# Optimization experiments

Measured on AMD Instinct MI355X. Metric: run time of the kernel, lower is better.

## Reference

```python
import jax, jax.numpy as jnp
import numpy as np

BITS = 32
HDC_DIM = 512
IN_SCALE = 23  # 1 + 2*input_window_size, window=11


def setup_inputs() -> dict:
    key = jax.random.key(0)
    k1, k2, k3, k4 = jax.random.split(key, 4)
    B = 2
    D = IN_SCALE * IN_SCALE  # 529
    num_nonzero = int(0.5 * D * HDC_DIM)  # 135424
    return {
        "data_input": jax.random.normal(k1, (B, 4 * IN_SCALE, IN_SCALE), dtype=jnp.float32),
        "structure_input": jax.random.normal(k2, (B, IN_SCALE, IN_SCALE), dtype=jnp.float32),
        "parameters_temp": jax.random.uniform(k3, (IN_SCALE, IN_SCALE), dtype=jnp.float32),
        "non_zero_indices": jax.random.randint(k4, (num_nonzero,), 0, D * HDC_DIM, dtype=jnp.int32),
    }


def _bit_unpack(x_float):
    # view float32 bits as int32, unpack into 0/1 per bit (little-endian bit order),
    # matching torch: x.unsqueeze(-1).bitwise_and(2**arange(bits)).ne(0)
    xi = jax.lax.bitcast_convert_type(x_float, jnp.int32)
    mask = jnp.left_shift(jnp.int32(1), jnp.arange(BITS, dtype=jnp.int32))  # [32], incl. sign bit
    return ((xi[..., None] & mask) != 0).astype(jnp.int32)  # [..., 32]


def reference(data_input, structure_input, parameters_temp, non_zero_indices):
    B = data_input.shape[0]
    n = IN_SCALE
    # channel slices
    r = data_input[:, 0:n, :].reshape(B, -1)            # [B, D]
    g = data_input[:, n:2 * n, :].reshape(B, -1)
    b = data_input[:, 2 * n:3 * n, :].reshape(B, -1)
    a = data_input[:, 3 * n:4 * n, :].reshape(B, -1)
    s = (structure_input * parameters_temp).reshape(B, -1)  # [B, D]
    D = r.shape[1]

    # sparse random scatter into flat projection buffer (faithful to torch semantics:
    # view(-1)[idx] = 1, then view(-1)[~idx] = 0 where ~idx indexes total-1-idx via negative wrap)
    total = B * D * BITS * HDC_DIM
    proj = jnp.zeros((total,), dtype=jnp.int32)
    proj = proj.at[non_zero_indices].set(1)
    proj = proj.at[total - 1 - non_zero_indices].set(0)
    proj = proj.reshape(B, D, BITS, HDC_DIM)

    # bit-unpack + broadcast-XOR against projection (no materialized repeat)
    r_bin = _bit_unpack(r)[..., None] ^ proj  # [B, D, 32, hdc]
    g_bin = _bit_unpack(g)[..., None] ^ proj
    b_bin = _bit_unpack(b)[..., None] ^ proj
    a_bin = _bit_unpack(a)[..., None] ^ proj
    s_bin = _bit_unpack(s)[..., None] ^ proj

    return (r, g, b, a, s, r_bin, g_bin, b_bin, a_bin, s_bin)
```

## Files before the change

kernel.cpp:

```cpp
#include <hip/hip_runtime.h>
#include <stdint.h>

#define DDIM 529
#define BATCH 2
#define BITS 32
#define HDC 512
#define ROW (BITS * HDC)
#define NNZ_REGION (DDIM * HDC)
#define SMALL (5 * BATCH * DDIM)
#define BIN_PER_OUT (BATCH * DDIM * ROW)
#define TOTAL_FLOATS (SMALL + 5 * BIN_PER_OUT)
#define Q_BEG 1323
#define Q_END (TOTAL_FLOATS / 4)

typedef float f32x4 __attribute__((ext_vector_type(4)));

__global__ void prep(const float* __restrict__ data,
                     const float* __restrict__ structure,
                     const float* __restrict__ params,
                     float* __restrict__ out, int* __restrict__ xw) {
    int i = blockIdx.x * blockDim.x + threadIdx.x;
    if (i >= SMALL) return;
    int c = i / 1058, rem = i % 1058, bb = rem / DDIM, d = rem % DDIM;
    float v = (c < 4) ? data[bb * (4 * DDIM) + c * DDIM + d]
                      : structure[bb * DDIM + d] * params[d];
    out[i] = v;
    unsigned x = (unsigned)__float_as_int(v);
    xw[i] = (int)x;
    if (i == 0) {
        float f = (float)(x & 1u);
        out[SMALL] = f; out[SMALL + 1] = f;
    }
    if (i == SMALL - 1) {
        float f = (float)(x >> 31);
        out[TOTAL_FLOATS - 2] = f; out[TOTAL_FLOATS - 1] = f;
    }
}

__global__ __launch_bounds__(256) void stream4(const int* __restrict__ xw,
                                               float* __restrict__ out) {
    const unsigned nt = gridDim.x * 256u;
    f32x4* o4 = (f32x4*)out;
    for (unsigned q = Q_BEG + blockIdx.x * 256u + threadIdx.x; q < Q_END; q += nt) {
        unsigned E0 = 4u * q - SMALL;
        unsigned E2 = E0 + 2u;
        unsigned w0 = (unsigned)xw[E0 >> 14];
        unsigned w1 = (unsigned)xw[E2 >> 14];
        float fa = (float)((w0 >> ((E0 & 16383u) >> 9)) & 1u);
        float fb = (float)((w1 >> ((E2 & 16383u) >> 9)) & 1u);
        f32x4 v = {fa, fa, fb, fb};
        o4[q] = v;
    }
}

__global__ void bins_fixup(const int* __restrict__ idx, int n,
                           const int* __restrict__ xw,
                           float* __restrict__ out) {
    int i = blockIdx.x * blockDim.x + threadIdx.x;
    if (i >= n) return;
    unsigned p = (unsigned)idx[i];
    if (p >= NNZ_REGION) return;
    unsigned d = p >> 14;
    unsigned j = (p >> 9) & 31u;
    #pragma unroll
    for (int c = 0; c < 5; ++c) {
        unsigned w = (unsigned)xw[c * 1058 + d];
        out[(size_t)SMALL + (size_t)c * BIN_PER_OUT + p] = (float)(((w >> j) & 1u) ^ 1u);
    }
}

extern "C" void kernel_launch(void* const* d_in, const int* in_sizes, int n_in,
                              void* d_out, int out_size, void* d_ws, size_t ws_size,
                              hipStream_t stream) {
    const float* data      = (const float*)d_in[0];
    const float* structure = (const float*)d_in[1];
    const float* params    = (const float*)d_in[2];
    const int*   nzi       = (const int*)d_in[3];
    int nnz = in_sizes[3];

    float* out = (float*)d_out;
    int*   xw  = (int*)d_ws;

    prep<<<(SMALL + 255) / 256, 256, 0, stream>>>(data, structure, params, out, xw);
    stream4<<<1024, 256, 0, stream>>>(xw, out);
    bins_fixup<<<(nnz + 255) / 256, 256, 0, stream>>>(nzi, nnz, xw, out);
}
```

Before: 81.44 us.

## Drop prep kernel, recompute bit words inline and merge small outputs into fixup

Removes the prep kernel and its workspace by having the streaming kernel and fixup kernel recompute each row's float bit pattern directly from the inputs. The small-output writes and edge bits move into the fixup kernel, cutting launches from three to two. The stream grid is doubled to 2048 blocks. The cost is extra divisions and gathers per element in the streaming loop, which are mostly cached since rows are large.

```diff
diff --git a/kernel.cpp b/kernel.cpp
--- a/kernel.cpp
+++ b/kernel.cpp
@@ -15,57 +15,71 @@
 
 typedef float f32x4 __attribute__((ext_vector_type(4)));
 
-__global__ void prep(const float* __restrict__ data,
-                     const float* __restrict__ structure,
-                     const float* __restrict__ params,
-                     float* __restrict__ out, int* __restrict__ xw) {
-    int i = blockIdx.x * blockDim.x + threadIdx.x;
-    if (i >= SMALL) return;
-    int c = i / 1058, rem = i % 1058, bb = rem / DDIM, d = rem % DDIM;
+__device__ __forceinline__ unsigned rowword(int r,
+                                            const float* __restrict__ data,
+                                            const float* __restrict__ structure,
+                                            const float* __restrict__ params) {
+    int c   = r / (BATCH * DDIM);
+    int rem = r - c * (BATCH * DDIM);
+    int bb  = rem / DDIM;
+    int d   = rem - bb * DDIM;
     float v = (c < 4) ? data[bb * (4 * DDIM) + c * DDIM + d]
                       : structure[bb * DDIM + d] * params[d];
-    out[i] = v;
-    unsigned x = (unsigned)__float_as_int(v);
-    xw[i] = (int)x;
-    if (i == 0) {
-        float f = (float)(x & 1u);
-        out[SMALL] = f; out[SMALL + 1] = f;
-    }
-    if (i == SMALL - 1) {
-        float f = (float)(x >> 31);
-        out[TOTAL_FLOATS - 2] = f; out[TOTAL_FLOATS - 1] = f;
-    }
+    return (unsigned)__float_as_int(v);
 }
 
-__global__ __launch_bounds__(256) void stream4(const int* __restrict__ xw,
+__global__ __launch_bounds__(256) void stream4(const float* __restrict__ data,
+                                               const float* __restrict__ structure,
+                                               const float* __restrict__ params,
                                                float* __restrict__ out) {
     const unsigned nt = gridDim.x * 256u;
     f32x4* o4 = (f32x4*)out;
     for (unsigned q = Q_BEG + blockIdx.x * 256u + threadIdx.x; q < Q_END; q += nt) {
         unsigned E0 = 4u * q - SMALL;
         unsigned E2 = E0 + 2u;
-        unsigned w0 = (unsigned)xw[E0 >> 14];
-        unsigned w1 = (unsigned)xw[E2 >> 14];
+        int r0 = (int)(E0 >> 14);
+        int r2 = (int)(E2 >> 14);
+        unsigned w0 = rowword(r0, data, structure, params);
+        unsigned w2 = (r2 == r0) ? w0 : rowword(r2, data, structure, params);
         float fa = (float)((w0 >> ((E0 & 16383u) >> 9)) & 1u);
-        float fb = (float)((w1 >> ((E2 & 16383u) >> 9)) & 1u);
+        float fb = (float)((w2 >> ((E2 & 16383u) >> 9)) & 1u);
         f32x4 v = {fa, fa, fb, fb};
         o4[q] = v;
     }
 }
 
-__global__ void bins_fixup(const int* __restrict__ idx, int n,
-                           const int* __restrict__ xw,
-                           float* __restrict__ out) {
+__global__ __launch_bounds__(256) void finalize(const int* __restrict__ idx, int n,
+                                                const float* __restrict__ data,
+                                                const float* __restrict__ structure,
+                                                const float* __restrict__ params,
+                                                float* __restrict__ out) {
     int i = blockIdx.x * blockDim.x + threadIdx.x;
-    if (i >= n) return;
-    unsigned p = (unsigned)idx[i];
-    if (p >= NNZ_REGION) return;
-    unsigned d = p >> 14;
-    unsigned j = (p >> 9) & 31u;
-    #pragma unroll
-    for (int c = 0; c < 5; ++c) {
-        unsigned w = (unsigned)xw[c * 1058 + d];
-        out[(size_t)SMALL + (size_t)c * BIN_PER_OUT + p] = (float)(((w >> j) & 1u) ^ 1u);
+
+    if (i < SMALL) {
+        unsigned w = rowword(i, data, structure, params);
+        out[i] = __int_as_float((int)w);
+        if (i == 0) {
+            float f = (float)(w & 1u);
+            out[SMALL] = f; out[SMALL + 1] = f;
+        }
+        if (i == SMALL - 1) {
+            float f = (float)(w >> 31);
+            out[TOTAL_FLOATS - 2] = f; out[TOTAL_FLOATS - 1] = f;
+        }
+    }
+
+    if (i < n) {
+        unsigned p = (unsigned)idx[i];
+        if (p < NNZ_REGION) {
+            unsigned d = p >> 14;
+            unsigned j = (p >> 9) & 31u;
+            #pragma unroll
+            for (int c = 0; c < 5; ++c) {
+                float v = (c < 4) ? data[c * DDIM + d] : structure[d] * params[d];
+                unsigned bit = ((unsigned)__float_as_int(v) >> j) & 1u;
+                out[(size_t)SMALL + (size_t)c * BIN_PER_OUT + p] = (float)(bit ^ 1u);
+            }
+        }
     }
 }
 
@@ -79,9 +93,7 @@
     int nnz = in_sizes[3];
 
     float* out = (float*)d_out;
-    int*   xw  = (int*)d_ws;
 
-    prep<<<(SMALL + 255) / 256, 256, 0, stream>>>(data, structure, params, out, xw);
-    stream4<<<1024, 256, 0, stream>>>(xw, out);
-    bins_fixup<<<(nnz + 255) / 256, 256, 0, stream>>>(nzi, nnz, xw, out);
+    stream4<<<2048, 256, 0, stream>>>(data, structure, params, out);
+    finalize<<<(nnz + 255) / 256, 256, 0, stream>>>(nzi, nnz, data, structure, params, out);
 }
```

New measurement: 83.81 us. +2.9%, slower.
